# Kernel tuning notes

Hardware: AMD Instinct MI355X
Metric: run time of the kernel (lower is better)

The kernel has to match this reference:

```python
import jax, jax.numpy as jnp
import numpy as np

B, S, C, L = 32, 256, 50, 20   # batch, max_seq_len, char_emb_dim, word_len
F, W = 30, 3                   # filter_num, char_window_size


def setup_inputs() -> dict:
    key = jax.random.key(0)
    k1, k2, k3 = jax.random.split(key, 3)
    char_embeddings_feature = jax.random.normal(k1, (B, S, C, L), dtype=jnp.float32)
    # torch grouped Conv1d weight: [out_ch=C*F, in_ch/groups=1, kernel=W]
    weight = jax.random.normal(k2, (C * F, 1, W), dtype=jnp.float32) * 0.1
    bias = jax.random.normal(k3, (C * F,), dtype=jnp.float32) * 0.1
    return {"char_embeddings_feature": char_embeddings_feature, "weight": weight, "bias": bias}


def reference(char_embeddings_feature, weight, bias):
    b, s, c, l = char_embeddings_feature.shape
    out_ch = weight.shape[0]
    # Fuse the per-position python loop: fold (batch, seq) into one conv batch dim.
    x = char_embeddings_feature.reshape(b * s, c, l)
    # Grouped (depthwise-style) conv: groups == c, each group has F output filters.
    y = jax.lax.conv_general_dilated(
        x, weight,
        window_strides=(1,), padding='VALID',
        dimension_numbers=('NCH', 'OIH', 'NCH'),
        feature_group_count=c,
    )  # [b*s, c*F, l-W+1]
    y = y + bias[None, :, None]
    # max-pool over conv output length, then restore (batch, seq)
    return y.max(axis=2).reshape(b, s, out_ch)
```

## Files before the change

### kernel.cpp

```cpp
#include <hip/hip_runtime.h>

constexpr int Bc = 32;
constexpr int Sc = 256;
constexpr int Cc = 50;
constexpr int Lc = 20;
constexpr int Fc = 30;
constexpr int Wc = 3;
constexpr int OUT_CH   = Cc * Fc;
constexpr int CONV_LEN = Lc - Wc + 1;
constexpr int XSZ      = Cc * Lc;
constexpr int BLOCK    = 256;
constexpr int CH_PER_T = 6;
constexpr int NP       = 4;
constexpr int ACT      = OUT_CH / CH_PER_T;

static __device__ __forceinline__ void block_sync() {
    asm volatile("s_waitcnt lgkmcnt(0)" ::: "memory");
    __builtin_amdgcn_s_barrier();
    asm volatile("" ::: "memory");
}

__global__ __launch_bounds__(BLOCK, 4)
void charcnn_kernel(const float* __restrict__ x,
                    const float* __restrict__ weight,
                    const float* __restrict__ bias,
                    float* __restrict__ out)
{
    __shared__ float xs[2][XSZ];

    const int t    = threadIdx.x;
    const int pos0 = blockIdx.x * NP;
    const bool on  = (t < ACT);

    float w[CH_PER_T * Wc];
    float bb[CH_PER_T];
    if (on) {
        const float2* wp = (const float2*)(weight + t * (CH_PER_T * Wc));
        #pragma unroll
        for (int i = 0; i < (CH_PER_T * Wc) / 2; ++i) {
            const float2 q = wp[i];
            w[2*i] = q.x; w[2*i+1] = q.y;
        }
        const float2* bp = (const float2*)(bias + t * CH_PER_T);
        #pragma unroll
        for (int i = 0; i < CH_PER_T / 2; ++i) {
            const float2 q = bp[i];
            bb[2*i] = q.x; bb[2*i+1] = q.y;
        }
    }

    const int c = t / 5;

    float4 preA, preB;
    if (on) {
        float4 s0 = ((const float4*)(x + (size_t)(pos0 + 0) * XSZ))[t];
        preA      = ((const float4*)(x + (size_t)(pos0 + 1) * XSZ))[t];
        ((float4*)xs[0])[t] = s0;
    }
    block_sync();

    #pragma unroll
    for (int p = 0; p < NP; ++p) {
        const int buf = p & 1;

        if (on && (p + 2 < NP))
            preB = ((const float4*)(x + (size_t)(pos0 + p + 2) * XSZ))[t];

        float res[CH_PER_T];
        if (on) {
            float v[Lc];
            const float4* rowv = (const float4*)(xs[buf] + c * Lc);
            #pragma unroll
            for (int i = 0; i < Lc / 4; ++i) {
                const float4 q = rowv[i];
                v[4*i+0] = q.x; v[4*i+1] = q.y; v[4*i+2] = q.z; v[4*i+3] = q.w;
            }

            #pragma unroll
            for (int j = 0; j < CH_PER_T; ++j) {
                const float w0 = w[3*j + 0];
                const float w1 = w[3*j + 1];
                const float w2 = w[3*j + 2];

                float m = fmaf(v[0], w0, fmaf(v[1], w1, v[2] * w2));
                #pragma unroll
                for (int q = 1; q + 1 < CONV_LEN; q += 2) {
                    const float a = fmaf(v[q],   w0, fmaf(v[q+1], w1, v[q+2] * w2));
                    const float b = fmaf(v[q+1], w0, fmaf(v[q+2], w1, v[q+3] * w2));
                    m = fmaxf(fmaxf(m, a), b);
                }
                const float a = fmaf(v[CONV_LEN-1], w0,
                                fmaf(v[CONV_LEN],   w1, v[CONV_LEN+1] * w2));
                m = fmaxf(m, a);

                res[j] = m + bb[j];
            }

            if (p + 1 < NP)
                ((float4*)xs[buf ^ 1])[t] = preA;

            float* op = out + (size_t)(pos0 + p) * OUT_CH + t * CH_PER_T;
            #pragma unroll
            for (int i = 0; i < CH_PER_T / 2; ++i)
                ((float2*)op)[i] = make_float2(res[2*i], res[2*i+1]);

            preA = preB;
        }

        if (p + 1 < NP) block_sync();
    }
}

extern "C" void kernel_launch(void* const* d_in, const int* in_sizes, int n_in,
                              void* d_out, int out_size, void* d_ws, size_t ws_size,
                              hipStream_t stream) {
    const float* x      = (const float*)d_in[0];
    const float* weight = (const float*)d_in[1];
    const float* bias   = (const float*)d_in[2];
    float* out          = (float*)d_out;

    const int nBlocks = (Bc * Sc) / NP;
    charcnn_kernel<<<nBlocks, BLOCK, 0, stream>>>(x, weight, bias, out);
}
```

Measured before the change: 29.27 us.

## Use 512-thread blocks with 3 channels per thread and 8 positions per block

Changes the work split so each thread computes 3 output channels instead of 6, with 500 active threads per 512-thread block. Each block now processes 8 positions instead of 4, which halves the grid. Staging into shared memory is done by a separate subset of 250 threads, and prefetch depth drops from two positions ahead to one. The aim is more parallelism per position and fewer registers per thread, at the cost of scalar (non-vector) output stores and weight loads, fewer blocks, and less prefetch lookahead.

```diff
diff --git a/kernel.cpp b/kernel.cpp
--- a/kernel.cpp
+++ b/kernel.cpp
@@ -9,10 +9,11 @@
 constexpr int OUT_CH   = Cc * Fc;
 constexpr int CONV_LEN = Lc - Wc + 1;
 constexpr int XSZ      = Cc * Lc;
-constexpr int BLOCK    = 256;
-constexpr int CH_PER_T = 6;
-constexpr int NP       = 4;
+constexpr int BLOCK    = 512;
+constexpr int CH_PER_T = 3;
+constexpr int NP       = 8;
 constexpr int ACT      = OUT_CH / CH_PER_T;
+constexpr int STG      = XSZ / 4;
 
 static __device__ __forceinline__ void block_sync() {
     asm volatile("s_waitcnt lgkmcnt(0)" ::: "memory");
@@ -20,7 +21,7 @@
     asm volatile("" ::: "memory");
 }
 
-__global__ __launch_bounds__(BLOCK, 4)
+__global__ __launch_bounds__(BLOCK, 8)
 void charcnn_kernel(const float* __restrict__ x,
                     const float* __restrict__ weight,
                     const float* __restrict__ bias,
@@ -31,51 +32,45 @@
     const int t    = threadIdx.x;
     const int pos0 = blockIdx.x * NP;
     const bool on  = (t < ACT);
+    const bool stg = (t < STG);
 
     float w[CH_PER_T * Wc];
     float bb[CH_PER_T];
     if (on) {
-        const float2* wp = (const float2*)(weight + t * (CH_PER_T * Wc));
+        const float* wp = weight + t * (CH_PER_T * Wc);
         #pragma unroll
-        for (int i = 0; i < (CH_PER_T * Wc) / 2; ++i) {
-            const float2 q = wp[i];
-            w[2*i] = q.x; w[2*i+1] = q.y;
-        }
-        const float2* bp = (const float2*)(bias + t * CH_PER_T);
+        for (int i = 0; i < CH_PER_T * Wc; ++i) w[i] = wp[i];
+        const float* bp = bias + t * CH_PER_T;
         #pragma unroll
-        for (int i = 0; i < CH_PER_T / 2; ++i) {
-            const float2 q = bp[i];
-            bb[2*i] = q.x; bb[2*i+1] = q.y;
-        }
+        for (int i = 0; i < CH_PER_T; ++i) bb[i] = bp[i];
     }
 
-    const int c = t / 5;
+    const int c = t / 10;
 
-    float4 preA, preB;
-    if (on) {
-        float4 s0 = ((const float4*)(x + (size_t)(pos0 + 0) * XSZ))[t];
-        preA      = ((const float4*)(x + (size_t)(pos0 + 1) * XSZ))[t];
-        ((float4*)xs[0])[t] = s0;
-    }
+    if (stg)
+        ((float4*)xs[0])[t] = ((const float4*)(x + (size_t)pos0 * XSZ))[t];
     block_sync();
 
-    #pragma unroll
+    #pragma unroll 2
     for (int p = 0; p < NP; ++p) {
         const int buf = p & 1;
 
-        if (on && (p + 2 < NP))
-            preB = ((const float4*)(x + (size_t)(pos0 + p + 2) * XSZ))[t];
+        float4 preA;
+        if (stg && (p + 1 < NP))
+            preA = ((const float4*)(x + (size_t)(pos0 + p + 1) * XSZ))[t];
 
-        float res[CH_PER_T];
         if (on) {
             float v[Lc];
-            const float4* rowv = (const float4*)(xs[buf] + c * Lc);
-            #pragma unroll
-            for (int i = 0; i < Lc / 4; ++i) {
-                const float4 q = rowv[i];
-                v[4*i+0] = q.x; v[4*i+1] = q.y; v[4*i+2] = q.z; v[4*i+3] = q.w;
+            {
+                const float4* rowv = (const float4*)(xs[buf] + c * Lc);
+                #pragma unroll
+                for (int i = 0; i < Lc / 4; ++i) {
+                    const float4 q = rowv[i];
+                    v[4*i+0] = q.x; v[4*i+1] = q.y; v[4*i+2] = q.z; v[4*i+3] = q.w;
+                }
             }
 
+            float* op = out + (size_t)(pos0 + p) * OUT_CH + t * CH_PER_T;
             #pragma unroll
             for (int j = 0; j < CH_PER_T; ++j) {
                 const float w0 = w[3*j + 0];
@@ -89,23 +84,15 @@
                     const float b = fmaf(v[q+1], w0, fmaf(v[q+2], w1, v[q+3] * w2));
                     m = fmaxf(fmaxf(m, a), b);
                 }
-                const float a = fmaf(v[CONV_LEN-1], w0,
-                                fmaf(v[CONV_LEN],   w1, v[CONV_LEN+1] * w2));
-                m = fmaxf(m, a);
+                m = fmaxf(m, fmaf(v[CONV_LEN-1], w0,
+                           fmaf(v[CONV_LEN],     w1, v[CONV_LEN+1] * w2)));
 
-                res[j] = m + bb[j];
+                op[j] = m + bb[j];
             }
+        }
 
-            if (p + 1 < NP)
-                ((float4*)xs[buf ^ 1])[t] = preA;
-
-            float* op = out + (size_t)(pos0 + p) * OUT_CH + t * CH_PER_T;
-            #pragma unroll
-            for (int i = 0; i < CH_PER_T / 2; ++i)
-                ((float2*)op)[i] = make_float2(res[2*i], res[2*i+1]);
-
-            preA = preB;
-        }
+        if (stg && (p + 1 < NP))
+            ((float4*)xs[buf ^ 1])[t] = preA;
 
         if (p + 1 < NP) block_sync();
     }
```

New measurement: 27.53 us. 1.06x faster.
